# Performance work log

Measured on AMD Instinct MI355X. Metric: run time of the kernel, lower is better.

Reference implementation:

```python
import jax, jax.numpy as jnp
import numpy as np

# snntorch atan surrogate spike (alpha=2): fwd heaviside, bwd 1/(1+(pi*x)^2)
@jax.custom_vjp
def atan_spike(x):
    return (x > 0).astype(x.dtype)

def _atan_fwd(x):
    return atan_spike(x), x

def _atan_bwd(x, g):
    return (g / (1.0 + (jnp.pi * x) ** 2),)

atan_spike.defvjp(_atan_fwd, _atan_bwd)

B, C, T, H, O = 2048, 5, 2048, 16, 2

def setup_inputs() -> dict:
    key = jax.random.key(0)
    ks = jax.random.split(key, 6)
    x = jax.random.normal(ks[0], (B, C, T), dtype=jnp.float32)
    conv_w = jax.random.normal(ks[1], (H, C, 3), dtype=jnp.float32) * (1.0 / np.sqrt(C * 3))
    conv_b = jax.random.normal(ks[2], (H,), dtype=jnp.float32) * 0.01
    bn_gamma = jnp.ones((H,), jnp.float32)
    bn_beta = jnp.zeros((H,), jnp.float32)
    bn_mean = jnp.zeros((H,), jnp.float32)   # BatchNorm1d running stats (eval mode)
    bn_var = jnp.ones((H,), jnp.float32)
    fc_w = jax.random.normal(ks[3], (O, H), dtype=jnp.float32) * (1.0 / np.sqrt(H))
    fc_b = jax.random.normal(ks[4], (O,), dtype=jnp.float32) * 0.01
    beta1 = jnp.float32(0.8)   # snn.Leaky learn_beta=True -> scalar param
    beta2 = jnp.float32(0.8)
    return dict(x=x, conv_w=conv_w, conv_b=conv_b, bn_gamma=bn_gamma, bn_beta=bn_beta,
                bn_mean=bn_mean, bn_var=bn_var, fc_w=fc_w, fc_b=fc_b,
                beta1=beta1, beta2=beta2)

def reference(x, conv_w, conv_b, bn_gamma, bn_beta, bn_mean, bn_var, fc_w, fc_b, beta1, beta2):
    EPS, THR = 1e-5, 1.0
    # Conv1d(k=3, pad=1) on a length-1 signal: only the middle tap contributes.
    w_mid = conv_w[:, :, 1]                      # [H, C]
    scale = bn_gamma / jnp.sqrt(bn_var + EPS)    # fold BN affine
    b1 = jnp.clip(beta1, 0.0, 1.0)               # snntorch clamps learned beta
    b2 = jnp.clip(beta2, 0.0, 1.0)
    xT = jnp.transpose(x, (2, 0, 1))             # [T, B, C]
    dt = x.dtype
    mem1_0 = jnp.zeros((x.shape[0], w_mid.shape[0]), dt)
    mem2_0 = jnp.zeros((x.shape[0], fc_w.shape[0]), dt)
    acc_0 = jnp.zeros_like(mem2_0)

    def step(carry, xt):
        mem1, mem2, acc = carry
        feat = (xt * 2.0) @ w_mid.T + conv_b                 # conv1d -> [B, H]
        feat = (feat - bn_mean) * scale + bn_beta            # BN (running stats)
        # snntorch Leaky (reset_mechanism='subtract'): reset from PREVIOUS mem, detached
        reset1 = jax.lax.stop_gradient((mem1 > THR).astype(dt))
        mem1 = b1 * mem1 + feat - reset1 * THR
        spk1 = atan_spike(mem1 - THR)
        cur2 = spk1 @ fc_w.T + fc_b                          # [B, O]
        reset2 = jax.lax.stop_gradient((mem2 > THR).astype(dt))
        mem2 = b2 * mem2 + cur2 - reset2 * THR
        spk2 = atan_spike(mem2 - THR)
        return (mem1, mem2, acc + spk2), None

    (_, _, acc), _ = jax.lax.scan(step, (mem1_0, mem2_0, acc_0), xT)
    return acc  # sum of output spikes over time, [B, num_classes]
```

## Files before the change

kernel.cpp:

```cpp
#include <hip/hip_runtime.h>
#include <type_traits>

typedef float v2f __attribute__((ext_vector_type(2)));

#define BB 2048
#define CC 5
#define TT 2048
#define HH 16
#define OO 2

#define NCH  32
#define CHT  (TT / NCH)
#define WARM 96
#define HP   8

#define TTL 32
#define BTL 256
#define XT_BYTES ((size_t)CC * TT * BB * 4)

__device__ __forceinline__ float comp4(const float4& v, int j) {
    return j == 0 ? v.x : (j == 1 ? v.y : (j == 2 ? v.z : v.w));
}
__device__ __forceinline__ v2f fma2(v2f a, v2f b, v2f c) {
    return __builtin_elementwise_fma(a, b, c);
}

__global__ __launch_bounds__(256) void transpose_kernel(
    const float* __restrict__ x, float* __restrict__ xT)
{
    __shared__ float tile[TTL][BTL + 1];
    const int c   = blockIdx.z;
    const int tb  = blockIdx.x * TTL;
    const int bb  = blockIdx.y * BTL;
    const int tid = threadIdx.x;

    const int s  = tid & 7;
    const int br = tid >> 3;
#pragma unroll
    for (int i = 0; i < 8; ++i) {
        const int b_local = br + i * 32;
        const float4 v = *reinterpret_cast<const float4*>(
            x + (size_t)(bb + b_local) * (CC * TT) + (size_t)c * TT + tb + 4 * s);
        tile[4 * s + 0][b_local] = v.x;
        tile[4 * s + 1][b_local] = v.y;
        tile[4 * s + 2][b_local] = v.z;
        tile[4 * s + 3][b_local] = v.w;
    }
    __syncthreads();

#pragma unroll
    for (int t = 0; t < TTL; ++t)
        xT[((size_t)c * TT + tb + t) * BB + bb + tid] = tile[t][tid];
}

__global__ __launch_bounds__(64, 1) void snn_scanT_kernel(
    const float* __restrict__ xT,
    const float* __restrict__ conv_w,
    const float* __restrict__ conv_b,
    const float* __restrict__ bn_gamma,
    const float* __restrict__ bn_beta,
    const float* __restrict__ bn_mean,
    const float* __restrict__ bn_var,
    const float* __restrict__ fc_w,
    const float* __restrict__ fc_b,
    const float* __restrict__ beta1p,
    const float* __restrict__ beta2p,
    float* __restrict__ out)
{
    const int b     = blockIdx.x * 64 + threadIdx.x;
    const int chunk = blockIdx.y;

    const float b1 = fminf(fmaxf(beta1p[0], 0.0f), 1.0f);
    const float b2 = fminf(fmaxf(beta2p[0], 0.0f), 1.0f);
    const v2f b1v = {b1, b1};

    v2f wp[CC][HP], effbp[HP], fw0p[HP], fw1p[HP];
#pragma unroll
    for (int hp = 0; hp < HP; ++hp) {
        {
            const int h = 2 * hp;
            const float sc = bn_gamma[h] * rsqrtf(bn_var[h] + 1e-5f);
#pragma unroll
            for (int c = 0; c < CC; ++c)
                wp[c][hp].x = 2.0f * conv_w[h * (CC * 3) + c * 3 + 1] * sc;
            effbp[hp].x = (conv_b[h] - bn_mean[h]) * sc + bn_beta[h];
            fw0p[hp].x = fc_w[h];
            fw1p[hp].x = fc_w[HH + h];
        }
        {
            const int h = 2 * hp + 1;
            const float sc = bn_gamma[h] * rsqrtf(bn_var[h] + 1e-5f);
#pragma unroll
            for (int c = 0; c < CC; ++c)
                wp[c][hp].y = 2.0f * conv_w[h * (CC * 3) + c * 3 + 1] * sc;
            effbp[hp].y = (conv_b[h] - bn_mean[h]) * sc + bn_beta[h];
            fw0p[hp].y = fc_w[h];
            fw1p[hp].y = fc_w[HH + h];
        }
    }
    const float fb0 = fc_b[0], fb1 = fc_b[1];

    const int t_start = chunk * CHT;
    int tw            = t_start - WARM;
    if (tw < 0) tw = 0;
    const int t_end   = t_start + CHT;
    const int ngroups = (t_end - tw) >> 2;
    const int warm_g  = (t_start - tw) >> 2;

    v2f mem1p[HP] = {}, sp[HP] = {};
    float mem2_0 = 0.0f, mem2_1 = 0.0f, s2f0 = 0.0f, s2f1 = 0.0f;
    float acc0 = 0.0f, acc1 = 0.0f;

    auto ldg = [&](float (&buf)[CC][4], int t) __attribute__((always_inline)) {
#pragma unroll
        for (int c = 0; c < CC; ++c)
#pragma unroll
            for (int j = 0; j < 4; ++j)
                buf[c][j] = xT[((size_t)c * TT + t + j) * BB + b];
    };

    float bufA[CC][4], bufB[CC][4], bufC[CC][4], bufD[CC][4];
    ldg(bufA, tw);
    ldg(bufB, tw + 4);
    ldg(bufC, tw + 8);
    ldg(bufD, tw + 12);

    auto step4 = [&](const float (&cur)[CC][4], auto ACCC) __attribute__((always_inline)) {
#pragma unroll
        for (int j = 0; j < 4; ++j) {
            v2f xv[CC];
#pragma unroll
            for (int c = 0; c < CC; ++c) {
                const float xs = cur[c][j];
                xv[c].x = xs; xv[c].y = xs;
            }

            v2f r0p = {0.0f, 0.0f}, r1p = {0.0f, 0.0f};
#pragma unroll
            for (int hp = 0; hp < HP; ++hp) {
                v2f f = effbp[hp];
#pragma unroll
                for (int c = 0; c < CC; ++c)
                    f = fma2(xv[c], wp[c][hp], f);

                const v2f m = fma2(b1v, mem1p[hp], f - sp[hp]);
                mem1p[hp] = m;
                v2f s;
                s.x = m.x > 1.0f ? 1.0f : 0.0f;
                s.y = m.y > 1.0f ? 1.0f : 0.0f;
                sp[hp] = s;
                r0p = fma2(s, fw0p[hp], r0p);
                r1p = fma2(s, fw1p[hp], r1p);
            }
            const float cur2_0 = r0p.x + r0p.y + fb0;
            const float cur2_1 = r1p.x + r1p.y + fb1;

            mem2_0 = fmaf(b2, mem2_0, cur2_0 - s2f0);
            s2f0 = mem2_0 > 1.0f ? 1.0f : 0.0f;
            mem2_1 = fmaf(b2, mem2_1, cur2_1 - s2f1);
            s2f1 = mem2_1 > 1.0f ? 1.0f : 0.0f;

            if constexpr (decltype(ACCC)::value) {
                acc0 += s2f0;
                acc1 += s2f1;
            }
        }
    };

    const int nquads = ngroups >> 2;
    const int wquads = warm_g >> 2;
    const int tlast  = t_end - 4;

#define RUN_QUAD(ACCC)                                                   \
    {                                                                    \
        int t0 = tw + (4 * q + 4) * 4; if (t0 > tlast) t0 = tlast;       \
        int t1 = tw + (4 * q + 5) * 4; if (t1 > tlast) t1 = tlast;       \
        int t2 = tw + (4 * q + 6) * 4; if (t2 > tlast) t2 = tlast;       \
        int t3 = tw + (4 * q + 7) * 4; if (t3 > tlast) t3 = tlast;       \
        step4(bufA, ACCC); ldg(bufA, t0);                                \
        step4(bufB, ACCC); ldg(bufB, t1);                                \
        step4(bufC, ACCC); ldg(bufC, t2);                                \
        step4(bufD, ACCC); ldg(bufD, t3);                                \
    }

#pragma unroll 1
    for (int q = 0; q < wquads; ++q)
        RUN_QUAD((std::integral_constant<bool, false>{}));
#pragma unroll 1
    for (int q = wquads; q < nquads; ++q)
        RUN_QUAD((std::integral_constant<bool, true>{}));
#undef RUN_QUAD

    atomicAdd(&out[(size_t)b * OO + 0], acc0);
    atomicAdd(&out[(size_t)b * OO + 1], acc1);
}

__global__ __launch_bounds__(64, 1) void snn_laneb_fb_kernel(
    const float* __restrict__ x,
    const float* __restrict__ conv_w,
    const float* __restrict__ conv_b,
    const float* __restrict__ bn_gamma,
    const float* __restrict__ bn_beta,
    const float* __restrict__ bn_mean,
    const float* __restrict__ bn_var,
    const float* __restrict__ fc_w,
    const float* __restrict__ fc_b,
    const float* __restrict__ beta1p,
    const float* __restrict__ beta2p,
    float* __restrict__ out)
{
    const int b     = blockIdx.x * 64 + threadIdx.x;
    const int chunk = blockIdx.y;

    const float b1 = fminf(fmaxf(beta1p[0], 0.0f), 1.0f);
    const float b2 = fminf(fmaxf(beta2p[0], 0.0f), 1.0f);
    const v2f b1v = {b1, b1};

    v2f wp[CC][HP], effbp[HP], fw0p[HP], fw1p[HP];
#pragma unroll
    for (int hp = 0; hp < HP; ++hp) {
        {
            const int h = 2 * hp;
            const float sc = bn_gamma[h] * rsqrtf(bn_var[h] + 1e-5f);
#pragma unroll
            for (int c = 0; c < CC; ++c)
                wp[c][hp].x = 2.0f * conv_w[h * (CC * 3) + c * 3 + 1] * sc;
            effbp[hp].x = (conv_b[h] - bn_mean[h]) * sc + bn_beta[h];
            fw0p[hp].x = fc_w[h];
            fw1p[hp].x = fc_w[HH + h];
        }
        {
            const int h = 2 * hp + 1;
            const float sc = bn_gamma[h] * rsqrtf(bn_var[h] + 1e-5f);
#pragma unroll
            for (int c = 0; c < CC; ++c)
                wp[c][hp].y = 2.0f * conv_w[h * (CC * 3) + c * 3 + 1] * sc;
            effbp[hp].y = (conv_b[h] - bn_mean[h]) * sc + bn_beta[h];
            fw0p[hp].y = fc_w[h];
            fw1p[hp].y = fc_w[HH + h];
        }
    }
    const float fb0 = fc_b[0], fb1 = fc_b[1];

    const float* xb = x + (size_t)b * CC * TT;

    const int t_start = chunk * CHT;
    int tw            = t_start - WARM;
    if (tw < 0) tw = 0;
    const int t_end   = t_start + CHT;
    const int ngroups = (t_end - tw) >> 2;
    const int warm_g  = (t_start - tw) >> 2;

    v2f mem1p[HP] = {}, sp[HP] = {};
    float mem2_0 = 0.0f, mem2_1 = 0.0f, s2f0 = 0.0f, s2f1 = 0.0f;
    float acc0 = 0.0f, acc1 = 0.0f;

    auto ldg = [&](float4 (&buf)[CC], int t) __attribute__((always_inline)) {
#pragma unroll
        for (int c = 0; c < CC; ++c)
            buf[c] = *reinterpret_cast<const float4*>(xb + c * TT + t);
    };

    float4 bufA[CC], bufB[CC], bufC[CC], bufD[CC];
    ldg(bufA, tw);
    ldg(bufB, tw + 4);
    ldg(bufC, tw + 8);
    ldg(bufD, tw + 12);

    auto step4 = [&](const float4 (&cur)[CC], auto ACCC) __attribute__((always_inline)) {
#pragma unroll
        for (int j = 0; j < 4; ++j) {
            v2f xv[CC];
#pragma unroll
            for (int c = 0; c < CC; ++c) {
                const float xs = comp4(cur[c], j);
                xv[c].x = xs; xv[c].y = xs;
            }
            v2f r0p = {0.0f, 0.0f}, r1p = {0.0f, 0.0f};
#pragma unroll
            for (int hp = 0; hp < HP; ++hp) {
                v2f f = effbp[hp];
#pragma unroll
                for (int c = 0; c < CC; ++c)
                    f = fma2(xv[c], wp[c][hp], f);
                const v2f m = fma2(b1v, mem1p[hp], f - sp[hp]);
                mem1p[hp] = m;
                v2f s;
                s.x = m.x > 1.0f ? 1.0f : 0.0f;
                s.y = m.y > 1.0f ? 1.0f : 0.0f;
                sp[hp] = s;
                r0p = fma2(s, fw0p[hp], r0p);
                r1p = fma2(s, fw1p[hp], r1p);
            }
            const float cur2_0 = r0p.x + r0p.y + fb0;
            const float cur2_1 = r1p.x + r1p.y + fb1;
            mem2_0 = fmaf(b2, mem2_0, cur2_0 - s2f0);
            s2f0 = mem2_0 > 1.0f ? 1.0f : 0.0f;
            mem2_1 = fmaf(b2, mem2_1, cur2_1 - s2f1);
            s2f1 = mem2_1 > 1.0f ? 1.0f : 0.0f;
            if constexpr (decltype(ACCC)::value) {
                acc0 += s2f0;
                acc1 += s2f1;
            }
        }
    };

    const int nquads = ngroups >> 2;
    const int wquads = warm_g >> 2;
    const int tlast  = t_end - 4;

#define RUN_QUAD(ACCC)                                                   \
    {                                                                    \
        int t0 = tw + (4 * q + 4) * 4; if (t0 > tlast) t0 = tlast;       \
        int t1 = tw + (4 * q + 5) * 4; if (t1 > tlast) t1 = tlast;       \
        int t2 = tw + (4 * q + 6) * 4; if (t2 > tlast) t2 = tlast;       \
        int t3 = tw + (4 * q + 7) * 4; if (t3 > tlast) t3 = tlast;       \
        step4(bufA, ACCC); ldg(bufA, t0);                                \
        step4(bufB, ACCC); ldg(bufB, t1);                                \
        step4(bufC, ACCC); ldg(bufC, t2);                                \
        step4(bufD, ACCC); ldg(bufD, t3);                                \
    }

#pragma unroll 1
    for (int q = 0; q < wquads; ++q)
        RUN_QUAD((std::integral_constant<bool, false>{}));
#pragma unroll 1
    for (int q = wquads; q < nquads; ++q)
        RUN_QUAD((std::integral_constant<bool, true>{}));
#undef RUN_QUAD

    atomicAdd(&out[(size_t)b * OO + 0], acc0);
    atomicAdd(&out[(size_t)b * OO + 1], acc1);
}

extern "C" void kernel_launch(void* const* d_in, const int* in_sizes, int n_in,
                              void* d_out, int out_size, void* d_ws, size_t ws_size,
                              hipStream_t stream) {
    const float* x        = (const float*)d_in[0];
    const float* conv_w   = (const float*)d_in[1];
    const float* conv_b   = (const float*)d_in[2];
    const float* bn_gamma = (const float*)d_in[3];
    const float* bn_beta  = (const float*)d_in[4];
    const float* bn_mean  = (const float*)d_in[5];
    const float* bn_var   = (const float*)d_in[6];
    const float* fc_w     = (const float*)d_in[7];
    const float* fc_b     = (const float*)d_in[8];
    const float* beta1    = (const float*)d_in[9];
    const float* beta2    = (const float*)d_in[10];
    float* out = (float*)d_out;

    hipMemsetAsync(out, 0, (size_t)out_size * sizeof(float), stream);

    if (ws_size >= XT_BYTES) {
        float* xT = (float*)d_ws;
        dim3 tgrid(TT / TTL, BB / BTL, CC);
        transpose_kernel<<<tgrid, 256, 0, stream>>>(x, xT);
        dim3 grid(BB / 64, NCH);
        snn_scanT_kernel<<<grid, dim3(64), 0, stream>>>(
            xT, conv_w, conv_b, bn_gamma, bn_beta, bn_mean, bn_var,
            fc_w, fc_b, beta1, beta2, out);
    } else {
        dim3 grid(BB / 64, NCH);
        snn_laneb_fb_kernel<<<grid, dim3(64), 0, stream>>>(
            x, conv_w, conv_b, bn_gamma, bn_beta, bn_mean, bn_var,
            fc_w, fc_b, beta1, beta2, out);
    }
}
```

Measured before the change: 93.84 us.

## Split hidden units across lane pairs and combine partial sums with DPP swap

The scan kernel now assigns each batch element to two adjacent lanes, each computing 8 of the 16 hidden neurons, which doubles the number of wavefronts in the grid. The layer-2 input current is formed by adding the partner lane's partial sum through a DPP quad-permute swap, and only even lanes write the result atomically. This aims to shorten the serial per-thread dependency chain and raise occupancy (launch bounds now allow 2 blocks). In exchange, the x loads are duplicated across the two lanes and each time step adds a cross-lane operation.

```diff
diff --git a/kernel.cpp b/kernel.cpp
--- a/kernel.cpp
+++ b/kernel.cpp
@@ -12,7 +12,6 @@
 #define NCH  32
 #define CHT  (TT / NCH)
 #define WARM 96
-#define HP   8
 
 #define TTL 32
 #define BTL 256
@@ -23,6 +22,10 @@
 }
 __device__ __forceinline__ v2f fma2(v2f a, v2f b, v2f c) {
     return __builtin_elementwise_fma(a, b, c);
+}
+__device__ __forceinline__ float qswap_add(float v) {
+    int s = __builtin_amdgcn_update_dpp(0, __float_as_int(v), 0xB1, 0xf, 0xf, true);
+    return v + __int_as_float(s);
 }
 
 __global__ __launch_bounds__(256) void transpose_kernel(
@@ -53,7 +56,7 @@
         xT[((size_t)c * TT + tb + t) * BB + bb + tid] = tile[t][tid];
 }
 
-__global__ __launch_bounds__(64, 1) void snn_scanT_kernel(
+__global__ __launch_bounds__(64, 2) void snn_scanT2_kernel(
     const float* __restrict__ xT,
     const float* __restrict__ conv_w,
     const float* __restrict__ conv_b,
@@ -67,18 +70,20 @@
     const float* __restrict__ beta2p,
     float* __restrict__ out)
 {
-    const int b     = blockIdx.x * 64 + threadIdx.x;
+    const int lane  = threadIdx.x;
+    const int b     = blockIdx.x * 32 + (lane >> 1);
+    const int hb    = (lane & 1) * 8;
     const int chunk = blockIdx.y;
 
     const float b1 = fminf(fmaxf(beta1p[0], 0.0f), 1.0f);
     const float b2 = fminf(fmaxf(beta2p[0], 0.0f), 1.0f);
     const v2f b1v = {b1, b1};
 
-    v2f wp[CC][HP], effbp[HP], fw0p[HP], fw1p[HP];
-#pragma unroll
-    for (int hp = 0; hp < HP; ++hp) {
+    v2f wp[CC][4], effbp[4], fw0p[4], fw1p[4];
+#pragma unroll
+    for (int hp = 0; hp < 4; ++hp) {
         {
-            const int h = 2 * hp;
+            const int h = hb + 2 * hp;
             const float sc = bn_gamma[h] * rsqrtf(bn_var[h] + 1e-5f);
 #pragma unroll
             for (int c = 0; c < CC; ++c)
@@ -88,7 +93,7 @@
             fw1p[hp].x = fc_w[HH + h];
         }
         {
-            const int h = 2 * hp + 1;
+            const int h = hb + 2 * hp + 1;
             const float sc = bn_gamma[h] * rsqrtf(bn_var[h] + 1e-5f);
 #pragma unroll
             for (int c = 0; c < CC; ++c)
@@ -107,7 +112,7 @@
     const int ngroups = (t_end - tw) >> 2;
     const int warm_g  = (t_start - tw) >> 2;
 
-    v2f mem1p[HP] = {}, sp[HP] = {};
+    v2f mem1p[4] = {}, sp[4] = {};
     float mem2_0 = 0.0f, mem2_1 = 0.0f, s2f0 = 0.0f, s2f1 = 0.0f;
     float acc0 = 0.0f, acc1 = 0.0f;
 
@@ -137,7 +142,7 @@
 
             v2f r0p = {0.0f, 0.0f}, r1p = {0.0f, 0.0f};
 #pragma unroll
-            for (int hp = 0; hp < HP; ++hp) {
+            for (int hp = 0; hp < 4; ++hp) {
                 v2f f = effbp[hp];
 #pragma unroll
                 for (int c = 0; c < CC; ++c)
@@ -152,8 +157,8 @@
                 r0p = fma2(s, fw0p[hp], r0p);
                 r1p = fma2(s, fw1p[hp], r1p);
             }
-            const float cur2_0 = r0p.x + r0p.y + fb0;
-            const float cur2_1 = r1p.x + r1p.y + fb1;
+            const float cur2_0 = qswap_add(r0p.x + r0p.y) + fb0;
+            const float cur2_1 = qswap_add(r1p.x + r1p.y) + fb1;
 
             mem2_0 = fmaf(b2, mem2_0, cur2_0 - s2f0);
             s2f0 = mem2_0 > 1.0f ? 1.0f : 0.0f;
@@ -191,8 +196,10 @@
         RUN_QUAD((std::integral_constant<bool, true>{}));
 #undef RUN_QUAD
 
-    atomicAdd(&out[(size_t)b * OO + 0], acc0);
-    atomicAdd(&out[(size_t)b * OO + 1], acc1);
+    if (!(lane & 1)) {
+        atomicAdd(&out[(size_t)b * OO + 0], acc0);
+        atomicAdd(&out[(size_t)b * OO + 1], acc1);
+    }
 }
 
 __global__ __launch_bounds__(64, 1) void snn_laneb_fb_kernel(
@@ -216,9 +223,9 @@
     const float b2 = fminf(fmaxf(beta2p[0], 0.0f), 1.0f);
     const v2f b1v = {b1, b1};
 
-    v2f wp[CC][HP], effbp[HP], fw0p[HP], fw1p[HP];
-#pragma unroll
-    for (int hp = 0; hp < HP; ++hp) {
+    v2f wp[CC][8], effbp[8], fw0p[8], fw1p[8];
+#pragma unroll
+    for (int hp = 0; hp < 8; ++hp) {
         {
             const int h = 2 * hp;
             const float sc = bn_gamma[h] * rsqrtf(bn_var[h] + 1e-5f);
@@ -251,7 +258,7 @@
     const int ngroups = (t_end - tw) >> 2;
     const int warm_g  = (t_start - tw) >> 2;
 
-    v2f mem1p[HP] = {}, sp[HP] = {};
+    v2f mem1p[8] = {}, sp[8] = {};
     float mem2_0 = 0.0f, mem2_1 = 0.0f, s2f0 = 0.0f, s2f1 = 0.0f;
     float acc0 = 0.0f, acc1 = 0.0f;
 
@@ -278,7 +285,7 @@
             }
             v2f r0p = {0.0f, 0.0f}, r1p = {0.0f, 0.0f};
 #pragma unroll
-            for (int hp = 0; hp < HP; ++hp) {
+            for (int hp = 0; hp < 8; ++hp) {
                 v2f f = effbp[hp];
 #pragma unroll
                 for (int c = 0; c < CC; ++c)
@@ -355,8 +362,8 @@
         float* xT = (float*)d_ws;
         dim3 tgrid(TT / TTL, BB / BTL, CC);
         transpose_kernel<<<tgrid, 256, 0, stream>>>(x, xT);
-        dim3 grid(BB / 64, NCH);
-        snn_scanT_kernel<<<grid, dim3(64), 0, stream>>>(
+        dim3 grid(BB / 32, NCH);
+        snn_scanT2_kernel<<<grid, dim3(64), 0, stream>>>(
             xT, conv_w, conv_b, bn_gamma, bn_beta, bn_mean, bn_var,
             fc_w, fc_b, beta1, beta2, out);
     } else {
```

Measured after the change: 225.3 us. 2.4x slower.
